# Performance work log

Hardware: AMD Instinct MI355X
Metric: run time of the kernel (lower is better)

Reference implementation:

```python
import jax, jax.numpy as jnp
import numpy as np

C, NH, NP = 512, 8, 4
HD = C // NH
H = W = D = 20
N = H * W * D
B = 2
EPS = 1e-5


def _layer_norm(x, g, b):
    mu = jnp.mean(x, axis=-1, keepdims=True)
    var = jnp.var(x, axis=-1, keepdims=True)
    return (x - mu) * jax.lax.rsqrt(var + EPS) * g + b


def setup_inputs() -> dict:
    key = jax.random.key(0)
    ks = jax.random.split(key, 10)

    def lin(k, fan_in, shape, scale=1.0):
        return (jax.random.normal(k, shape, jnp.float32) / np.float32(np.sqrt(fan_in))) * scale

    return {
        "f_query": jax.random.normal(ks[0], (B, C, H, W, D), jnp.float32),
        "f_kv": jax.random.normal(ks[1], (B, C, H, W, D), jnp.float32),
        "ln_g": jnp.ones((C,), jnp.float32),
        "ln_b": jnp.zeros((C,), jnp.float32),
        "Wq": lin(ks[2], C, (C, C)),
        "bq": jnp.zeros((C,), jnp.float32),
        "Wo1": lin(ks[3], C, (C, C)),
        "bo1": jnp.zeros((C,), jnp.float32),
        "Wo2": lin(ks[4], C, (C, NH * NP * 3), 0.1),  # small nonzero so interpolation is exercised
        "bo2": jnp.zeros((NH * NP * 3,), jnp.float32),
        "Wa": lin(ks[5], C, (C, NH * NP)),
        "ba": jnp.zeros((NH * NP,), jnp.float32),
        "Wout": lin(ks[6], C, (C, C)),
        "bout": jnp.zeros((C,), jnp.float32),
    }


def reference(f_query, f_kv, ln_g, ln_b, Wq, bq, Wo1, bo1, Wo2, bo2, Wa, ba, Wout, bout):
    # tokens: flatten (H,W,D) in row-major order, matching torch .flatten(2)
    fq = jnp.transpose(f_query.reshape(B, C, N), (0, 2, 1))  # (B,N,C)
    q = _layer_norm(fq, ln_g, ln_b)
    Q = q @ Wq + bq  # (B,N,C)

    off = jnp.clip(jax.nn.relu(Q @ Wo1 + bo1) @ Wo2 + bo2, -3.0, 3.0)
    off = off.reshape(B, N, NH, NP, 3)
    attn = jax.nn.softmax((Q @ Wa + ba).reshape(B, N, NH, NP), axis=-1)

    gy, gx, gz = jnp.meshgrid(jnp.arange(H, dtype=jnp.float32),
                              jnp.arange(W, dtype=jnp.float32),
                              jnp.arange(D, dtype=jnp.float32), indexing='ij')
    base = jnp.stack([gy, gx, gz], -1).reshape(N, 3)  # (N,3) in (y,x,z)
    locs = base[None, :, None, None, :] + off         # (B,N,NH,NP,3)

    # normalization exactly as original module (ch0 by H, ch1 by W, ch2 by D)
    n0 = 2.0 * locs[..., 0] / (H - 1) - 1.0
    n1 = 2.0 * locs[..., 1] / (W - 1) - 1.0
    n2 = 2.0 * locs[..., 2] / (D - 1) - 1.0
    # torch grid_sample on input permuted to (B,c,D,H,W): grid ch0->x (W axis),
    # ch1->y (H axis), ch2->z (D axis); align_corners=True; border padding = clip
    ix = jnp.clip((n0 + 1.0) * 0.5 * (W - 1), 0.0, W - 1)
    iy = jnp.clip((n1 + 1.0) * 0.5 * (H - 1), 0.0, H - 1)
    iz = jnp.clip((n2 + 1.0) * 0.5 * (D - 1), 0.0, D - 1)

    x0 = jnp.floor(ix); y0 = jnp.floor(iy); z0 = jnp.floor(iz)
    fx = (ix - x0)[..., None]; fy = (iy - y0)[..., None]; fz = (iz - z0)[..., None]
    x0i = x0.astype(jnp.int32); y0i = y0.astype(jnp.int32); z0i = z0.astype(jnp.int32)
    x1i = jnp.minimum(x0i + 1, W - 1)
    y1i = jnp.minimum(y0i + 1, H - 1)
    z1i = jnp.minimum(z0i + 1, D - 1)

    # f_kv (B,C,H,W,D) -> per-head channels-last volume (B,NH,D,H,W,HD)
    feats = jnp.transpose(f_kv.reshape(B, NH, HD, H, W, D), (0, 1, 5, 3, 4, 2))
    bi = jnp.arange(B)[:, None, None, None]
    hi = jnp.arange(NH)[None, None, :, None]

    def g(zi, yi, xi):
        return feats[bi, hi, zi, yi, xi]  # (B,N,NH,NP,HD)

    sampled = (
        g(z0i, y0i, x0i) * (1 - fz) * (1 - fy) * (1 - fx)
        + g(z0i, y0i, x1i) * (1 - fz) * (1 - fy) * fx
        + g(z0i, y1i, x0i) * (1 - fz) * fy * (1 - fx)
        + g(z0i, y1i, x1i) * (1 - fz) * fy * fx
        + g(z1i, y0i, x0i) * fz * (1 - fy) * (1 - fx)
        + g(z1i, y0i, x1i) * fz * (1 - fy) * fx
        + g(z1i, y1i, x0i) * fz * fy * (1 - fx)
        + g(z1i, y1i, x1i) * fz * fy * fx
    )  # (B,N,NH,NP,HD)

    out = jnp.einsum('bnhp,bnhpc->bnhc', attn, sampled).reshape(B, N, C)
    out = out @ Wout + bout
    return jnp.transpose(out, (0, 2, 1)).reshape(B, C, H, W, D)
```

## Files before the change

kernel.cpp:

```cpp
#include <hip/hip_runtime.h>
#include <math.h>

#define C_DIM 512
#define NHEAD 8
#define HDIM 64
#define NTOK 8000
#define BN_TOK 16000

typedef __attribute__((ext_vector_type(8))) _Float16 f16x8;
typedef __attribute__((ext_vector_type(4))) float f32x4;
typedef __attribute__((ext_vector_type(2))) _Float16 h2;
typedef unsigned short u16;

__device__ __forceinline__ int imin(int a, int b) { return a < b ? a : b; }

__device__ __forceinline__ u16 f2h(float x) {
    _Float16 h = (_Float16)x;
    return __builtin_bit_cast(u16, h);
}

__device__ __forceinline__ size_t aidx(int t, int c) {
    return ((size_t)(t >> 4)) * 8192 + (size_t)((c >> 5) * 512
         + (((c >> 3) & 3) * 128) + ((t & 15) * 8) + (c & 7));
}
__device__ __forceinline__ size_t bidx(int n, int k) {
    return ((size_t)(n >> 4)) * 8192 + (size_t)((k >> 5) * 512
         + (((k >> 3) & 3) * 128) + ((n & 15) * 8) + (k & 7));
}

__device__ __forceinline__ void async16(const void* g, void* l) {
    __builtin_amdgcn_global_load_lds(
        (const __attribute__((address_space(1))) void*)g,
        (__attribute__((address_space(3))) void*)l, 16, 0, 0);
}

__device__ __forceinline__ f32x4 agload16(const u16* p) {
    f32x4 r;
    asm volatile("global_load_dwordx4 %0, %1, off" : "=v"(r) : "v"(p));
    return r;
}

#define VMWAIT(N) do { asm volatile("s_waitcnt vmcnt(" #N ")"); \
                       __builtin_amdgcn_sched_barrier(0); } while (0)

__global__ __launch_bounds__(256) void transpose_c2l_f16(
    const float* __restrict__ in, u16* __restrict__ out)
{
    __shared__ float tile[32][33];
    int b = blockIdx.z;
    const float* inb = in + (size_t)b * 512 * NTOK;
    u16* outb = out + (size_t)b * NTOK * 512;
    int s0 = blockIdx.x * 32, r0 = blockIdx.y * 32;
    int tx = threadIdx.x & 31, ty = threadIdx.x >> 5;
#pragma unroll
    for (int i = 0; i < 4; i++)
        tile[ty + i * 8][tx] = inb[(size_t)(r0 + ty + i * 8) * NTOK + s0 + tx];
    __syncthreads();
    int rq = threadIdx.x & 7, sy = threadIdx.x >> 3;
    ushort4 o;
    o.x = f2h(tile[rq * 4 + 0][sy]);
    o.y = f2h(tile[rq * 4 + 1][sy]);
    o.z = f2h(tile[rq * 4 + 2][sy]);
    o.w = f2h(tile[rq * 4 + 3][sy]);
    *reinterpret_cast<ushort4*>(outb + (size_t)(s0 + sy) * 512 + r0 + rq * 4) = o;
}

__global__ __launch_bounds__(256) void wcvt_all(
    const float* __restrict__ W0, u16* __restrict__ T0,
    const float* __restrict__ W1, u16* __restrict__ T1,
    const float* __restrict__ W2, u16* __restrict__ T2,
    const float* __restrict__ W3, u16* __restrict__ T3,
    const float* __restrict__ W4, u16* __restrict__ T4)
{
    const float* W; u16* Wt; int Nout, Npad;
    switch (blockIdx.z) {
        case 0: W = W0; Wt = T0; Nout = 512; Npad = 512; break;
        case 1: W = W1; Wt = T1; Nout = 512; Npad = 512; break;
        case 2: W = W2; Wt = T2; Nout = 512; Npad = 512; break;
        case 3: W = W3; Wt = T3; Nout = 96;  Npad = 128; break;
        default: W = W4; Wt = T4; Nout = 32; Npad = 128; break;
    }
    int blocked = (blockIdx.z != 2);
    int n0 = blockIdx.x * 32, k0 = blockIdx.y * 32;
    if (n0 >= Npad) return;
    __shared__ float t[32][33];
    int tx = threadIdx.x & 31, ty = threadIdx.x >> 5;
#pragma unroll
    for (int i = 0; i < 4; i++) {
        int k = k0 + ty + i * 8, n = n0 + tx;
        t[ty + i * 8][tx] = (n < Nout) ? W[(size_t)k * Nout + n] : 0.f;
    }
    __syncthreads();
#pragma unroll
    for (int i = 0; i < 4; i++) {
        int n = n0 + ty + i * 8, k = k0 + tx;
        u16 v = f2h(t[tx][ty + i * 8]);
        if (blocked) Wt[bidx(n, k)] = v;
        else         Wt[(size_t)n * 512 + k] = v;
    }
}

__device__ __forceinline__ void lds_gemm(
    const u16* Tin, u16* Tout, const u16* __restrict__ Wblk,
    const float* __restrict__ bias, int relu, int lane, int wv)
{
    int ml = lane & 15, quad = lane >> 4;
    int tg = wv & 3, ch = wv >> 2;
    const u16* Arow = Tin + (tg * 16 + ml) * 520;
#pragma unroll 1
    for (int cg = 0; cg < 4; ++cg) {
        int c0 = ch * 256 + cg * 64;
        const u16* Bp = Wblk + (size_t)(c0 >> 4) * 8192 + (size_t)lane * 8;
        f32x4 acc[4];
#pragma unroll
        for (int j = 0; j < 4; j++) acc[j] = (f32x4){0.f, 0.f, 0.f, 0.f};
        f32x4 bfr[4][4];
#pragma unroll
        for (int kb = 0; kb < 3; kb++)
#pragma unroll
            for (int j = 0; j < 4; j++)
                bfr[kb][j] = agload16(Bp + (size_t)j * 8192 + kb * 512);
#pragma unroll
        for (int kk = 0; kk < 16; kk++) {
            if (kk + 3 < 16) {
#pragma unroll
                for (int j = 0; j < 4; j++)
                    bfr[(kk + 3) & 3][j] = agload16(
                        Bp + (size_t)j * 8192 + (kk + 3) * 512);
            }
            f16x8 af = *reinterpret_cast<const f16x8*>(
                Arow + (kk * 4 + quad) * 8);
            if (kk < 13)       VMWAIT(12);
            else if (kk == 13) VMWAIT(8);
            else if (kk == 14) VMWAIT(4);
            else               VMWAIT(0);
#pragma unroll
            for (int j = 0; j < 4; j++)
                acc[j] = __builtin_amdgcn_mfma_f32_16x16x32_f16(
                    af, __builtin_bit_cast(f16x8, bfr[kk & 3][j]),
                    acc[j], 0, 0, 0);
        }
#pragma unroll
        for (int j = 0; j < 4; j++) {
            int col = c0 + j * 16 + ml;
            float bia = bias[col];
#pragma unroll
            for (int rg = 0; rg < 4; rg++) {
                float v = acc[j][rg] + bia;
                if (relu) v = fmaxf(v, 0.f);
                Tout[(tg * 16 + quad * 4 + rg) * 520 + col] = f2h(v);
            }
        }
    }
}

__global__ __launch_bounds__(512, 2) void mlp_fused(
    const float* __restrict__ fq, const float* __restrict__ gamma,
    const float* __restrict__ beta,
    const u16* __restrict__ Wqb, const float* __restrict__ bq,
    const u16* __restrict__ Wo1b, const float* __restrict__ bo1,
    const u16* __restrict__ Wo2b, const float* __restrict__ bo2,
    const u16* __restrict__ Wab, const float* __restrict__ ba,
    float* __restrict__ offb, float* __restrict__ lgb)
{
    __shared__ u16 T0[64 * 520], T1[64 * 520];
    __shared__ float ps[64][8], pq[64][8];
    __shared__ float muA[64], rsA[64];
    int tid = threadIdx.x, lane = tid & 63, wv = tid >> 6;
    int blk = blockIdx.x;
    int b = blk >= 125;
    int n0 = (blk - b * 125) * 64;
    int tp = tid & 63;
    const float* src = fq + (size_t)b * C_DIM * NTOK + n0 + tp;

    {
        float s = 0.f, q = 0.f;
#pragma unroll 8
        for (int it = 0; it < 64; ++it) {
            float v = src[(size_t)(it * 8 + wv) * NTOK];
            s += v; q += v * v;
        }
        ps[tp][wv] = s; pq[tp][wv] = q;
    }
    __syncthreads();
    if (tid < 64) {
        float S = 0.f, SQ = 0.f;
#pragma unroll
        for (int g = 0; g < 8; ++g) { S += ps[tid][g]; SQ += pq[tid][g]; }
        float mu = S * (1.f / 512.f);
        muA[tid] = mu;
        rsA[tid] = rsqrtf(SQ * (1.f / 512.f) - mu * mu + 1e-5f);
    }
    __syncthreads();
    {
        float mu = muA[tp], rs = rsA[tp];
#pragma unroll 8
        for (int it = 0; it < 64; ++it) {
            int c = it * 8 + wv;
            float v = src[(size_t)c * NTOK];
            T0[tp * 520 + c] = f2h((v - mu) * rs * gamma[c] + beta[c]);
        }
    }
    __syncthreads();
    lds_gemm(T0, T1, Wqb, bq, 0, lane, wv);
    __syncthreads();
    lds_gemm(T1, T0, Wo1b, bo1, 1, lane, wv);
    __syncthreads();
    {
        int ml = lane & 15, quad = lane >> 4;
        int isLg = wv >= 6;
        int cb = isLg ? (wv - 6) : wv;
        const u16* Tin = isLg ? T1 : T0;
        const u16* Wsm = isLg ? Wab : Wo2b;
        const float* bs = isLg ? ba : bo2;
        float* outg = isLg ? lgb : offb;
        int ldo = isLg ? 32 : 96;
        const u16* Wp = Wsm + (size_t)cb * 8192 + (size_t)lane * 8;
        f16x8 wb[16];
#pragma unroll
        for (int kk = 0; kk < 16; kk++)
            wb[kk] = *reinterpret_cast<const f16x8*>(Wp + (size_t)kk * 512);
        float bia = bs[cb * 16 + ml];
        int tbase = blk * 64;
#pragma unroll 1
        for (int tg = 0; tg < 4; tg++) {
            f32x4 acc = (f32x4){0.f, 0.f, 0.f, 0.f};
            const u16* Ar = Tin + (tg * 16 + ml) * 520;
#pragma unroll
            for (int kk = 0; kk < 16; kk++) {
                f16x8 af = *reinterpret_cast<const f16x8*>(
                    Ar + (kk * 4 + quad) * 8);
                acc = __builtin_amdgcn_mfma_f32_16x16x32_f16(
                    af, wb[kk], acc, 0, 0, 0);
            }
#pragma unroll
            for (int rg = 0; rg < 4; rg++)
                outg[(size_t)(tbase + tg * 16 + quad * 4 + rg) * ldo
                     + cb * 16 + ml] = acc[rg] + bia;
        }
    }
}

__device__ __forceinline__ void ws_body512(
    const u16* __restrict__ A, const u16* __restrict__ Bp,
    const float* __restrict__ bias, float* __restrict__ Cf,
    int colBase, int mt)
{
    __shared__ u16 Bs[64 * 512];
    int tid = threadIdx.x, lane = tid & 63, wv = tid >> 6;

#pragma unroll
    for (int c = 0; c < 8; c++) {
        int id = c * 512 + tid;
        int row = id >> 6, seg = id & 63;
        async16(Bp + (size_t)row * 512 + ((seg ^ (row & 7)) << 3),
                Bs + (size_t)id * 8);
    }

    int ml = lane & 15, quad = lane >> 4;
    int wm = (wv >> 1) * 64, wn = (wv & 1) * 32;

    int rowj[2];
#pragma unroll
    for (int j = 0; j < 2; j++) rowj[j] = wn + j * 16 + ml;

    __syncthreads();

    int bm = mt * 256;
    const u16* Ap = A + ((size_t)((bm + wm) >> 4)) * 8192 + (size_t)lane * 8;

    f32x4 acc[4][2];
#pragma unroll
    for (int i = 0; i < 4; i++)
#pragma unroll
        for (int j = 0; j < 2; j++) acc[i][j] = (f32x4){0.f, 0.f, 0.f, 0.f};

    f32x4 afr[4][4];
    f16x8 bf[2][2];

#pragma unroll
    for (int kb = 0; kb < 3; kb++)
#pragma unroll
        for (int i = 0; i < 4; i++)
            afr[kb][i] = agload16(Ap + (size_t)i * 8192 + kb * 512);
#pragma unroll
    for (int j = 0; j < 2; j++)
        bf[0][j] = *reinterpret_cast<const f16x8*>(
            Bs + (size_t)rowj[j] * 512 + (((0 + quad) ^ (rowj[j] & 7)) << 3));

#pragma unroll
    for (int kk = 0; kk < 16; kk++) {
        if (kk + 3 < 16) {
#pragma unroll
            for (int i = 0; i < 4; i++)
                afr[(kk + 3) & 3][i] = agload16(
                    Ap + (size_t)i * 8192 + (kk + 3) * 512);
        }
        if (kk + 1 < 16) {
#pragma unroll
            for (int j = 0; j < 2; j++) {
                int seg = (kk + 1) * 4 + quad;
                bf[(kk + 1) & 1][j] = *reinterpret_cast<const f16x8*>(
                    Bs + (size_t)rowj[j] * 512 + ((seg ^ (rowj[j] & 7)) << 3));
            }
        }
        if (kk < 13)       VMWAIT(12);
        else if (kk == 13) VMWAIT(8);
        else if (kk == 14) VMWAIT(4);
        else               VMWAIT(0);
#pragma unroll
        for (int i = 0; i < 4; i++)
#pragma unroll
            for (int j = 0; j < 2; j++)
                acc[i][j] = __builtin_amdgcn_mfma_f32_16x16x32_f16(
                    __builtin_bit_cast(f16x8, afr[kk & 3][i]),
                    bf[kk & 1][j], acc[i][j], 0, 0, 0);
    }

#pragma unroll
    for (int i = 0; i < 4; i++) {
        int row = bm + wm + i * 16 + quad * 4;
        if (row >= BN_TOK) continue;
#pragma unroll
        for (int j = 0; j < 2; j++) {
            int col = colBase + wn + j * 16 + ml;
            float bia = bias[col];
            int bb = row >= 8000;
            float4 st;
            st.x = acc[i][j][0] + bia;
            st.y = acc[i][j][1] + bia;
            st.z = acc[i][j][2] + bia;
            st.w = acc[i][j][3] + bia;
            *reinterpret_cast<float4*>(
                Cf + ((size_t)(bb * 512 + col)) * 8000 + (row - bb * 8000)) = st;
        }
    }
}

__global__ __launch_bounds__(512, 4) void gemm_out(
    const u16* __restrict__ A, const u16* __restrict__ WT,
    const float* __restrict__ bias, float* __restrict__ Cf)
{
    int did = blockIdx.x;
    int m = ((did >> 6) << 3) | (did & 7);
    if (m >= 63) return;
    int p = (did >> 3) & 7;
    ws_body512(A, WT + (size_t)p * 64 * 512, bias, Cf, p * 64, m);
}

__global__ __launch_bounds__(256) void sample_kernel(
    const u16* __restrict__ vol, const float* __restrict__ offb,
    const float* __restrict__ lgb, u16* __restrict__ outp)
{
    int wid = threadIdx.x >> 6, lane = threadIdx.x & 63;
    int bx = blockIdx.x;
    int bn = ((bx & 7) * 500 + (bx >> 3)) * 4 + wid;
    int h = lane >> 3, cl = lane & 7;
    int b = bn / NTOK, n = bn - b * NTOK;
    int y = n / 400;
    int r2 = n - y * 400;
    int x = r2 / 20;
    int z = r2 - x * 20;

    const float* op = offb + (size_t)bn * 96 + h * 12;
    const float* lp = lgb + (size_t)bn * 32 + h * 4;
    float l0 = lp[0], l1 = lp[1], l2 = lp[2], l3 = lp[3];
    float mx = fmaxf(fmaxf(l0, l1), fmaxf(l2, l3));
    float e0 = expf(l0 - mx), e1 = expf(l1 - mx), e2 = expf(l2 - mx), e3 = expf(l3 - mx);
    float inv = 1.f / (e0 + e1 + e2 + e3);
    float at[4] = {e0 * inv, e1 * inv, e2 * inv, e3 * inv};

    const u16* volb = vol + b * (NTOK * C_DIM) + h * HDIM + cl * 8;
    h2 acc0 = (h2)(_Float16)0, acc1 = acc0, acc2 = acc0, acc3 = acc0;
#pragma unroll 1
    for (int p = 0; p < 4; p++) {
        float o0 = fminf(fmaxf(op[p * 3 + 0], -3.f), 3.f);
        float o1 = fminf(fmaxf(op[p * 3 + 1], -3.f), 3.f);
        float o2 = fminf(fmaxf(op[p * 3 + 2], -3.f), 3.f);
        float ix = fminf(fmaxf((float)y + o0, 0.f), 19.f);
        float iy = fminf(fmaxf((float)x + o1, 0.f), 19.f);
        float iz = fminf(fmaxf((float)z + o2, 0.f), 19.f);
        float xf = floorf(ix), yf = floorf(iy), zf = floorf(iz);
        float fx = ix - xf, fy = iy - yf, fz = iz - zf;
        int x0 = (int)xf, y0 = (int)yf, z0 = (int)zf;
        int x1 = imin(x0 + 1, 19), y1 = imin(y0 + 1, 19), z1 = imin(z0 + 1, 19);
        int s00 = y0 * 400 + x0 * 20, s01 = y0 * 400 + x1 * 20;
        int s10 = y1 * 400 + x0 * 20, s11 = y1 * 400 + x1 * 20;
        uint4 v000 = *(const uint4*)(volb + (s00 + z0) * C_DIM);
        uint4 v001 = *(const uint4*)(volb + (s01 + z0) * C_DIM);
        uint4 v010 = *(const uint4*)(volb + (s10 + z0) * C_DIM);
        uint4 v011 = *(const uint4*)(volb + (s11 + z0) * C_DIM);
        uint4 v100 = *(const uint4*)(volb + (s00 + z1) * C_DIM);
        uint4 v101 = *(const uint4*)(volb + (s01 + z1) * C_DIM);
        uint4 v110 = *(const uint4*)(volb + (s10 + z1) * C_DIM);
        uint4 v111 = *(const uint4*)(volb + (s11 + z1) * C_DIM);
        float wz0 = (1.f - fz) * at[p], wz1 = fz * at[p];
        float w00 = wz0 * (1.f - fy), w01 = wz0 * fy;
        float w10 = wz1 * (1.f - fy), w11 = wz1 * fy;
        float gx0 = 1.f - fx;
        float cw[8] = { w00 * gx0, w00 * fx, w01 * gx0, w01 * fx,
                        w10 * gx0, w10 * fx, w11 * gx0, w11 * fx };
        const uint4* cv[8] = { &v000, &v001, &v010, &v011,
                               &v100, &v101, &v110, &v111 };
#pragma unroll
        for (int c = 0; c < 8; c++) {
            _Float16 wh = (_Float16)cw[c];
            h2 w2; w2.x = wh; w2.y = wh;
            uint4 d = *cv[c];
            acc0 += __builtin_bit_cast(h2, d.x) * w2;
            acc1 += __builtin_bit_cast(h2, d.y) * w2;
            acc2 += __builtin_bit_cast(h2, d.z) * w2;
            acc3 += __builtin_bit_cast(h2, d.w) * w2;
        }
    }
    uint4 o;
    o.x = __builtin_bit_cast(unsigned, acc0);
    o.y = __builtin_bit_cast(unsigned, acc1);
    o.z = __builtin_bit_cast(unsigned, acc2);
    o.w = __builtin_bit_cast(unsigned, acc3);
    *reinterpret_cast<uint4*>(outp + aidx(bn, h * HDIM + cl * 8)) = o;
}

extern "C" void kernel_launch(void* const* d_in, const int* in_sizes, int n_in,
                              void* d_out, int out_size, void* d_ws, size_t ws_size,
                              hipStream_t stream)
{
    const float* f_query = (const float*)d_in[0];
    const float* f_kv    = (const float*)d_in[1];
    const float* ln_g    = (const float*)d_in[2];
    const float* ln_b    = (const float*)d_in[3];
    const float* Wq      = (const float*)d_in[4];
    const float* bq      = (const float*)d_in[5];
    const float* Wo1     = (const float*)d_in[6];
    const float* bo1     = (const float*)d_in[7];
    const float* Wo2     = (const float*)d_in[8];
    const float* bo2     = (const float*)d_in[9];
    const float* Wa      = (const float*)d_in[10];
    const float* ba      = (const float*)d_in[11];
    const float* Wout    = (const float*)d_in[12];
    const float* bout    = (const float*)d_in[13];
    float* out = (float*)d_out;

    float* ws = (float*)d_ws;
    float* offb = ws;
    float* lgb  = ws + 1536000;
    u16* kvT   = (u16*)(ws + 2048000);
    u16* qb    = kvT  + 8192000;
    u16* WqT   = qb   + 8192000;
    u16* Wo1T  = WqT + 262144;
    u16* WoutT = Wo1T + 262144;
    u16* Wo2T  = WoutT + 262144;
    u16* WaT   = Wo2T + 65536;

    dim3 blk(256);
    dim3 blk512(512);
    wcvt_all<<<dim3(16, 16, 5), blk, 0, stream>>>(
        Wq, WqT, Wo1, Wo1T, Wout, WoutT, Wo2, Wo2T, Wa, WaT);
    transpose_c2l_f16<<<dim3(250, 16, 2), blk, 0, stream>>>(f_kv, kvT);
    mlp_fused<<<dim3(250), blk512, 0, stream>>>(
        f_query, ln_g, ln_b, WqT, bq, Wo1T, bo1, Wo2T, bo2, WaT, ba,
        offb, lgb);
    sample_kernel<<<dim3(4000), blk, 0, stream>>>(kvT, offb, lgb, qb);
    gemm_out<<<dim3(512), blk512, 0, stream>>>(qb, WoutT, bout, out);
}
```

Baseline: 215.7 us.

## Shrink mlp_fused token tile to 32 and retile LDS GEMM per wave

The fused MLP kernel now handles 32 tokens per block instead of 64 and launches 500 blocks instead of 250. Each wave covers a 64-column slice for both 16-token row groups, so every weight fragment loaded feeds two MFMAs, and the B-operand prefetch ring drops from depth 4 to 3. Halving the LDS footprint and raising launch_bounds to 4 blocks per CU aims for more blocks per CU and better fill across the GPU's compute units. The layernorm staging also writes 8 halves at a time as vector stores. In exchange, the whole weight set is streamed from global/L2 twice as many times, and the lower register budget may cause spills.

```diff
diff --git a/kernel.cpp b/kernel.cpp
--- a/kernel.cpp
+++ b/kernel.cpp
@@ -100,61 +100,68 @@
     }
 }
 
-__device__ __forceinline__ void lds_gemm(
+__device__ __forceinline__ void lds_gemm32(
     const u16* Tin, u16* Tout, const u16* __restrict__ Wblk,
     const float* __restrict__ bias, int relu, int lane, int wv)
 {
     int ml = lane & 15, quad = lane >> 4;
-    int tg = wv & 3, ch = wv >> 2;
-    const u16* Arow = Tin + (tg * 16 + ml) * 520;
-#pragma unroll 1
-    for (int cg = 0; cg < 4; ++cg) {
-        int c0 = ch * 256 + cg * 64;
-        const u16* Bp = Wblk + (size_t)(c0 >> 4) * 8192 + (size_t)lane * 8;
-        f32x4 acc[4];
-#pragma unroll
-        for (int j = 0; j < 4; j++) acc[j] = (f32x4){0.f, 0.f, 0.f, 0.f};
-        f32x4 bfr[4][4];
-#pragma unroll
-        for (int kb = 0; kb < 3; kb++)
+    int c0 = wv * 64;
+    const u16* Bp = Wblk + (size_t)(c0 >> 4) * 8192 + (size_t)lane * 8;
+    const u16* Ar0 = Tin + ml * 520;
+    const u16* Ar1 = Tin + (16 + ml) * 520;
+
+    f32x4 acc[2][4];
+#pragma unroll
+    for (int t = 0; t < 2; t++)
+#pragma unroll
+        for (int j = 0; j < 4; j++) acc[t][j] = (f32x4){0.f, 0.f, 0.f, 0.f};
+
+    f32x4 bfr[3][4];
+#pragma unroll
+    for (int kb = 0; kb < 2; kb++)
+#pragma unroll
+        for (int j = 0; j < 4; j++)
+            bfr[kb][j] = agload16(Bp + (size_t)j * 8192 + kb * 512);
+
+#pragma unroll
+    for (int kk = 0; kk < 16; kk++) {
+        if (kk + 2 < 16) {
 #pragma unroll
             for (int j = 0; j < 4; j++)
-                bfr[kb][j] = agload16(Bp + (size_t)j * 8192 + kb * 512);
-#pragma unroll
-        for (int kk = 0; kk < 16; kk++) {
-            if (kk + 3 < 16) {
-#pragma unroll
-                for (int j = 0; j < 4; j++)
-                    bfr[(kk + 3) & 3][j] = agload16(
-                        Bp + (size_t)j * 8192 + (kk + 3) * 512);
-            }
-            f16x8 af = *reinterpret_cast<const f16x8*>(
-                Arow + (kk * 4 + quad) * 8);
-            if (kk < 13)       VMWAIT(12);
-            else if (kk == 13) VMWAIT(8);
-            else if (kk == 14) VMWAIT(4);
-            else               VMWAIT(0);
-#pragma unroll
-            for (int j = 0; j < 4; j++)
-                acc[j] = __builtin_amdgcn_mfma_f32_16x16x32_f16(
-                    af, __builtin_bit_cast(f16x8, bfr[kk & 3][j]),
-                    acc[j], 0, 0, 0);
-        }
+                bfr[(kk + 2) % 3][j] = agload16(
+                    Bp + (size_t)j * 8192 + (kk + 2) * 512);
+        }
+        f16x8 a0 = *reinterpret_cast<const f16x8*>(Ar0 + (kk * 4 + quad) * 8);
+        f16x8 a1 = *reinterpret_cast<const f16x8*>(Ar1 + (kk * 4 + quad) * 8);
+        if (kk < 14)       VMWAIT(8);
+        else if (kk == 14) VMWAIT(4);
+        else               VMWAIT(0);
+#pragma unroll
+        for (int j = 0; j < 4; j++) {
+            f16x8 bj = __builtin_bit_cast(f16x8, bfr[kk % 3][j]);
+            acc[0][j] = __builtin_amdgcn_mfma_f32_16x16x32_f16(
+                a0, bj, acc[0][j], 0, 0, 0);
+            acc[1][j] = __builtin_amdgcn_mfma_f32_16x16x32_f16(
+                a1, bj, acc[1][j], 0, 0, 0);
+        }
+    }
+
+#pragma unroll
+    for (int t = 0; t < 2; t++)
 #pragma unroll
         for (int j = 0; j < 4; j++) {
             int col = c0 + j * 16 + ml;
             float bia = bias[col];
 #pragma unroll
             for (int rg = 0; rg < 4; rg++) {
-                float v = acc[j][rg] + bia;
+                float v = acc[t][j][rg] + bia;
                 if (relu) v = fmaxf(v, 0.f);
-                Tout[(tg * 16 + quad * 4 + rg) * 520 + col] = f2h(v);
+                Tout[(t * 16 + quad * 4 + rg) * 520 + col] = f2h(v);
             }
         }
-    }
-}
-
-__global__ __launch_bounds__(512, 2) void mlp_fused(
+}
+
+__global__ __launch_bounds__(512, 4) void mlp_fused(
     const float* __restrict__ fq, const float* __restrict__ gamma,
     const float* __restrict__ beta,
     const u16* __restrict__ Wqb, const float* __restrict__ bq,
@@ -163,30 +170,35 @@
     const u16* __restrict__ Wab, const float* __restrict__ ba,
     float* __restrict__ offb, float* __restrict__ lgb)
 {
-    __shared__ u16 T0[64 * 520], T1[64 * 520];
-    __shared__ float ps[64][8], pq[64][8];
-    __shared__ float muA[64], rsA[64];
+    __shared__ u16 T0[32 * 520], T1[32 * 520];
+    __shared__ float ps[32][17], pq[32][17];
+    __shared__ float muA[32], rsA[32];
     int tid = threadIdx.x, lane = tid & 63, wv = tid >> 6;
     int blk = blockIdx.x;
-    int b = blk >= 125;
-    int n0 = (blk - b * 125) * 64;
-    int tp = tid & 63;
+    int tp = tid & 31;
+    int cg = tid >> 5;
+    int b = blk >= 250;
+    int n0 = (blk - b * 250) * 32;
     const float* src = fq + (size_t)b * C_DIM * NTOK + n0 + tp;
 
     {
         float s = 0.f, q = 0.f;
-#pragma unroll 8
-        for (int it = 0; it < 64; ++it) {
-            float v = src[(size_t)(it * 8 + wv) * NTOK];
-            s += v; q += v * v;
-        }
-        ps[tp][wv] = s; pq[tp][wv] = q;
-    }
-    __syncthreads();
-    if (tid < 64) {
+#pragma unroll
+        for (int it = 0; it < 4; ++it) {
+            int c0 = (cg + it * 16) * 8;
+#pragma unroll
+            for (int e = 0; e < 8; ++e) {
+                float v = src[(size_t)(c0 + e) * NTOK];
+                s += v; q += v * v;
+            }
+        }
+        ps[tp][cg] = s; pq[tp][cg] = q;
+    }
+    __syncthreads();
+    if (tid < 32) {
         float S = 0.f, SQ = 0.f;
 #pragma unroll
-        for (int g = 0; g < 8; ++g) { S += ps[tid][g]; SQ += pq[tid][g]; }
+        for (int g = 0; g < 16; ++g) { S += ps[tid][g]; SQ += pq[tid][g]; }
         float mu = S * (1.f / 512.f);
         muA[tid] = mu;
         rsA[tid] = rsqrtf(SQ * (1.f / 512.f) - mu * mu + 1e-5f);
@@ -194,17 +206,23 @@
     __syncthreads();
     {
         float mu = muA[tp], rs = rsA[tp];
-#pragma unroll 8
-        for (int it = 0; it < 64; ++it) {
-            int c = it * 8 + wv;
-            float v = src[(size_t)c * NTOK];
-            T0[tp * 520 + c] = f2h((v - mu) * rs * gamma[c] + beta[c]);
-        }
-    }
-    __syncthreads();
-    lds_gemm(T0, T1, Wqb, bq, 0, lane, wv);
-    __syncthreads();
-    lds_gemm(T1, T0, Wo1b, bo1, 1, lane, wv);
+#pragma unroll
+        for (int it = 0; it < 4; ++it) {
+            int c0 = (cg + it * 16) * 8;
+            u16 o[8];
+#pragma unroll
+            for (int e = 0; e < 8; ++e) {
+                float v = src[(size_t)(c0 + e) * NTOK];
+                o[e] = f2h((v - mu) * rs * gamma[c0 + e] + beta[c0 + e]);
+            }
+            *reinterpret_cast<f16x8*>(&T0[tp * 520 + c0]) =
+                *reinterpret_cast<const f16x8*>(o);
+        }
+    }
+    __syncthreads();
+    lds_gemm32(T0, T1, Wqb, bq, 0, lane, wv);
+    __syncthreads();
+    lds_gemm32(T1, T0, Wo1b, bo1, 1, lane, wv);
     __syncthreads();
     {
         int ml = lane & 15, quad = lane >> 4;
@@ -221,9 +239,9 @@
         for (int kk = 0; kk < 16; kk++)
             wb[kk] = *reinterpret_cast<const f16x8*>(Wp + (size_t)kk * 512);
         float bia = bs[cb * 16 + ml];
-        int tbase = blk * 64;
-#pragma unroll 1
-        for (int tg = 0; tg < 4; tg++) {
+        int tbase = blk * 32;
+#pragma unroll
+        for (int tg = 0; tg < 2; tg++) {
             f32x4 acc = (f32x4){0.f, 0.f, 0.f, 0.f};
             const u16* Ar = Tin + (tg * 16 + ml) * 520;
 #pragma unroll
@@ -457,7 +475,7 @@
     wcvt_all<<<dim3(16, 16, 5), blk, 0, stream>>>(
         Wq, WqT, Wo1, Wo1T, Wout, WoutT, Wo2, Wo2T, Wa, WaT);
     transpose_c2l_f16<<<dim3(250, 16, 2), blk, 0, stream>>>(f_kv, kvT);
-    mlp_fused<<<dim3(250), blk512, 0, stream>>>(
+    mlp_fused<<<dim3(500), blk512, 0, stream>>>(
         f_query, ln_g, ln_b, WqT, bq, Wo1T, bo1, Wo2T, bo2, WaT, ba,
         offb, lgb);
     sample_kernel<<<dim3(4000), blk, 0, stream>>>(kvT, offb, lgb, qb);
```

Measured after the change: 202.8 us. 1.06x faster.
